# Kernel tuning notes

Hardware: AMD Instinct MI355X
Metric: run time of the kernel (lower is better)

## Reference

```python
import jax, jax.numpy as jnp
import numpy as np

ETA = 1.0
BETA = 0.6
LN_EPS = 1e-5


def layer_norm(x, scale, bias):
    mu = x.mean(-1, keepdims=True)
    var = ((x - mu) ** 2).mean(-1, keepdims=True)
    return (x - mu) / jnp.sqrt(var + LN_EPS) * scale + bias


def setup_inputs() -> dict:
    B, N, S, C, D = 8, 2048, 16, 32, 128
    key = jax.random.key(0)
    ks = jax.random.split(key, 10)
    X_short = jax.random.normal(ks[0], (B, N, S, C), dtype=jnp.float32)
    # binary temporal validity mask (float, as multiplied in the original)
    mask_short = (jax.random.uniform(ks[1], (B, N, S)) > 0.3).astype(jnp.float32)
    A_stat = jax.random.uniform(ks[2], (N, N), dtype=jnp.float32)
    M_mask = jax.random.randint(ks[3], (N, N), 0, 2).astype(jnp.int32)
    M_mask = M_mask.at[jnp.arange(N), jnp.arange(N)].set(1)  # keep self-edges so no all-masked row
    node_reliab = jax.random.uniform(ks[4], (B, N), dtype=jnp.float32)
    # learned parameters (stored (in, out) so application is x @ W)
    W_proj = jax.random.normal(ks[5], (C, D), dtype=jnp.float32) / np.sqrt(C)
    Wq = jax.random.normal(ks[6], (D, D), dtype=jnp.float32) / np.sqrt(D)
    Wk = jax.random.normal(ks[7], (D, D), dtype=jnp.float32) / np.sqrt(D)
    W_lin = jax.random.normal(ks[8], (D, D), dtype=jnp.float32) / np.sqrt(D)
    ln1_scale = jnp.ones((D,), jnp.float32)
    ln1_bias = jnp.zeros((D,), jnp.float32)
    ln2_scale = jnp.ones((D,), jnp.float32)
    ln2_bias = jnp.zeros((D,), jnp.float32)
    return {
        "X_short": X_short, "mask_short": mask_short, "A_stat": A_stat,
        "M_mask": M_mask, "node_reliab": node_reliab,
        "W_proj": W_proj, "Wq": Wq, "Wk": Wk, "W_lin": W_lin,
        "ln1_scale": ln1_scale, "ln1_bias": ln1_bias,
        "ln2_scale": ln2_scale, "ln2_bias": ln2_bias,
    }


def reference(X_short, mask_short, A_stat, M_mask, node_reliab,
              W_proj, Wq, Wk, W_lin, ln1_scale, ln1_bias, ln2_scale, ln2_bias):
    D = W_proj.shape[1]
    # masked temporal mean pooling over S
    denom = jnp.maximum(mask_short.sum(axis=2, keepdims=True), 1.0)      # (B,N,1)
    x = (X_short * mask_short[..., None]).sum(axis=2) / denom            # (B,N,C)
    Hn = x @ W_proj                                                      # (B,N,D)
    # dynamic graph attention
    Q = Hn @ Wq
    K = Hn @ Wk
    logits = jnp.einsum('bnd,bmd->bnm', Q, K) / jnp.sqrt(jnp.float32(D))
    p = jnp.clip(A_stat, 1e-3, 1.0 - 1e-3)
    bias = jnp.log(p / (1.0 - p))                                        # logit
    logits = logits + ETA * bias[None]
    edge = (M_mask != 0)[None]                                           # (1,N,N)
    logits = jnp.where(edge, logits, -jnp.inf)
    Adyn = jax.nn.softmax(logits, axis=-1)                               # (B,N,N)
    # fuse with static adjacency, reliability scaling, mask, row-renormalize
    A_fuse = BETA * Adyn + (1.0 - BETA) * A_stat[None]
    r = jnp.clip(node_reliab, 0.0, 1.0)                                  # (B,N)
    A_fuse = A_fuse * r[:, :, None] * r[:, None, :]
    A_fuse = A_fuse * M_mask.astype(A_fuse.dtype)[None]
    A_fuse = A_fuse / (A_fuse.sum(axis=-1, keepdims=True) + 1e-8)
    # propagate: A @ H -> linear -> relu -> (dropout=eval identity) -> LN -> outer LN
    H = jnp.einsum('bnm,bmd->bnd', A_fuse, Hn)
    H = H @ W_lin
    H = layer_norm(jax.nn.relu(H), ln1_scale, ln1_bias)
    out = layer_norm(H, ln2_scale, ln2_bias)
    return out, A_fuse
```

## Files before the change

### kernel.cpp

```cpp
#include <hip/hip_runtime.h>
#include <math.h>

#define BB 8
#define NN 2048
#define SS 16
#define CC 32
#define DD 128

typedef unsigned short u16;
typedef __attribute__((ext_vector_type(8))) short bf16x8;
typedef __attribute__((ext_vector_type(4))) float f32x4;

__device__ inline u16 f2bf(float f) {
    union { float f; unsigned u; } c; c.f = f;
    unsigned r = c.u + 0x7fff + ((c.u >> 16) & 1);
    return (u16)(r >> 16);
}
__device__ inline float bf2f(u16 h) {
    union { unsigned u; float f; } c; c.u = ((unsigned)h) << 16;
    return c.f;
}
__device__ inline u16 f2h(float f) {
    union { _Float16 h; u16 u; } c; c.h = (_Float16)f;
    return c.u;
}
__device__ inline float h2f(u16 u) {
    union { _Float16 h; u16 v; } c; c.v = u;
    return (float)c.h;
}
__device__ inline float clamp01(float v) { return fminf(fmaxf(v, 0.f), 1.f); }

__global__ __launch_bounds__(256) void prep_kernel(const float* __restrict__ Astat,
                                                   const int* __restrict__ Mm,
                                                   const float* __restrict__ Wproj,
                                                   const float* __restrict__ Wq,
                                                   const float* __restrict__ Wk,
                                                   const float* __restrict__ Wl,
                                                   u16* __restrict__ lgh,
                                                   u16* __restrict__ am,
                                                   float* __restrict__ Wpq,
                                                   float* __restrict__ Wpk,
                                                   u16* __restrict__ WlT) {
    int bx = blockIdx.x;
    if (bx < 4096) {
        size_t g = ((size_t)bx * 256 + threadIdx.x) * 4;
        float4 a4 = *(const float4*)&Astat[g];
        int4 m4 = *(const int4*)&Mm[g];
        float a[4] = {a4.x, a4.y, a4.z, a4.w};
        int mm[4] = {m4.x, m4.y, m4.z, m4.w};
        ushort4 lo, ao;
        u16 lg[4], ab[4];
#pragma unroll
        for (int j = 0; j < 4; ++j) {
            float p = fminf(fmaxf(a[j], 1e-3f), 1.f - 1e-3f);
            float l = __logf(p / (1.f - p));
            lg[j] = mm[j] ? f2h(l) : (u16)0xFC00;
            ab[j] = mm[j] ? f2bf(a[j]) : (u16)0;
        }
        lo.x = lg[0]; lo.y = lg[1]; lo.z = lg[2]; lo.w = lg[3];
        ao.x = ab[0]; ao.y = ab[1]; ao.z = ab[2]; ao.w = ab[3];
        *(ushort4*)&lgh[g] = lo;
        *(ushort4*)&am[g] = ao;
    } else if (bx < 4128) {
        int i = (bx - 4096) * 256 + threadIdx.x;
        int d = i & 127;
        int c = (i >> 7) & 31;
        int mat = i >> 12;
        const float* Wt = mat ? Wk : Wq;
        float acc = 0.f;
#pragma unroll 4
        for (int e = 0; e < DD; ++e)
            acc = fmaf(Wproj[c * DD + e], Wt[e * DD + d], acc);
        (mat ? Wpk : Wpq)[c * DD + d] = acc;
    } else {
        int i = (bx - 4128) * 256 + threadIdx.x;
        int dp = i >> 7, d = i & 127;
        WlT[dp * DD + d] = f2bf(Wl[d * DD + dp]);
    }
}

__global__ __launch_bounds__(256) void proj3_kernel(const float* __restrict__ X,
                                                    const float* __restrict__ Msk,
                                                    const float* __restrict__ Wproj,
                                                    const float* __restrict__ Wpq,
                                                    const float* __restrict__ Wpk,
                                                    u16* __restrict__ HnT,
                                                    u16* __restrict__ Qb,
                                                    u16* __restrict__ Kb) {
    __shared__ float wp[CC * DD], wq[CC * DD], wk[CC * DD];
    __shared__ float xs[CC * 36];
    int t = threadIdx.x;
    for (int i = t; i < CC * DD; i += 256) {
        wp[i] = Wproj[i];
        wq[i] = Wpq[i];
        wk[i] = Wpk[i];
    }
    int rbase = blockIdx.x * 32;
    {
        int row = t >> 3, cg = t & 7;
        const float* xrow = X + ((size_t)(rbase + row) * SS) * CC + cg * 4;
        const float* mrow = Msk + (size_t)(rbase + row) * SS;
        float4 acc = make_float4(0.f, 0.f, 0.f, 0.f);
        float msum = 0.f;
#pragma unroll
        for (int s = 0; s < SS; ++s) {
            float mv = mrow[s];
            float4 xv = *(const float4*)&xrow[s * CC];
            msum += mv;
            acc.x = fmaf(xv.x, mv, acc.x);
            acc.y = fmaf(xv.y, mv, acc.y);
            acc.z = fmaf(xv.z, mv, acc.z);
            acc.w = fmaf(xv.w, mv, acc.w);
        }
        float inv = 1.f / fmaxf(msum, 1.0f);
        xs[(cg * 4 + 0) * 36 + row] = acc.x * inv;
        xs[(cg * 4 + 1) * 36 + row] = acc.y * inv;
        xs[(cg * 4 + 2) * 36 + row] = acc.z * inv;
        xs[(cg * 4 + 3) * 36 + row] = acc.w * inv;
    }
    __syncthreads();

    int col = t & 127;
    int g = t >> 7;
    float ah[16], aq[16], ak[16];
#pragma unroll
    for (int i = 0; i < 16; ++i) { ah[i] = 0.f; aq[i] = 0.f; ak[i] = 0.f; }

#pragma unroll 4
    for (int k = 0; k < CC; ++k) {
        float wpv = wp[k * DD + col], wqv = wq[k * DD + col], wkv = wk[k * DD + col];
        const float4* xp = (const float4*)&xs[k * 36 + g * 16];
        float4 a0 = xp[0], a1 = xp[1], a2 = xp[2], a3 = xp[3];
        float xv[16] = {a0.x, a0.y, a0.z, a0.w, a1.x, a1.y, a1.z, a1.w,
                        a2.x, a2.y, a2.z, a2.w, a3.x, a3.y, a3.z, a3.w};
#pragma unroll
        for (int i = 0; i < 16; ++i) {
            ah[i] = fmaf(xv[i], wpv, ah[i]);
            aq[i] = fmaf(xv[i], wqv, aq[i]);
            ak[i] = fmaf(xv[i], wkv, ak[i]);
        }
    }
    const float scale = 0.08838834764831845f;
#pragma unroll
    for (int i = 0; i < 16; ++i) {
        size_t row = (size_t)(rbase + g * 16 + i);
        Qb[row * DD + col] = f2bf(aq[i] * scale);
        Kb[row * DD + col] = f2bf(ak[i]);
    }
    int b = rbase >> 11;
    int n0 = (rbase & (NN - 1)) + g * 16;
    u16* hp = HnT + (size_t)b * DD * NN + (size_t)col * NN + n0;
    unsigned pk[8];
#pragma unroll
    for (int i = 0; i < 8; ++i)
        pk[i] = (unsigned)f2bf(ah[2 * i]) | ((unsigned)f2bf(ah[2 * i + 1]) << 16);
    *(uint4*)&hp[0] = make_uint4(pk[0], pk[1], pk[2], pk[3]);
    *(uint4*)&hp[8] = make_uint4(pk[4], pk[5], pk[6], pk[7]);
}

#define LQT 136
__global__ __launch_bounds__(256) void stats_kernel(
        const u16* __restrict__ Qb, const u16* __restrict__ Kb,
        const u16* __restrict__ lgh, const u16* __restrict__ am,
        const float* __restrict__ rel,
        u16* __restrict__ Ebuf, float* __restrict__ part) {
    __shared__ u16 Qs[32 * LQT];
    __shared__ u16 Ks[128 * LQT];
    __shared__ float redE[128], redR[128], redA[128];
    int cs = blockIdx.x, rt = blockIdx.y, b = blockIdx.z;
    int R0 = rt * 32, C0 = cs * 512;
    int t = threadIdx.x;
    int lane = t & 63, w = t >> 6, q = lane >> 4, r16 = lane & 15;

    const u16* Qg = Qb + ((size_t)b * NN + R0) * DD;
#pragma unroll
    for (int rep = 0; rep < 2; ++rep) {
        int e = rep * 256 + t;
        int row = e >> 4, seg = e & 15;
        *(uint4*)&Qs[row * LQT + seg * 8] = *(const uint4*)&Qg[row * DD + seg * 8];
    }
    const u16* Kg = Kb + (size_t)b * NN * DD;
    float ER[2][4], LR[2][4], LA[2][4];
#pragma unroll
    for (int i = 0; i < 2; ++i)
#pragma unroll
        for (int r = 0; r < 4; ++r) { ER[i][r] = 0.f; LR[i][r] = 0.f; LA[i][r] = 0.f; }

    for (int ct = 0; ct < 4; ++ct) {
        __syncthreads();
#pragma unroll
        for (int rep = 0; rep < 8; ++rep) {
            int e = rep * 256 + t;
            int colr = e >> 4, seg = e & 15;
            *(uint4*)&Ks[colr * LQT + seg * 8] =
                *(const uint4*)&Kg[(size_t)(C0 + ct * 128 + colr) * DD + seg * 8];
        }
        __syncthreads();
        f32x4 acc[2][2];
#pragma unroll
        for (int i = 0; i < 2; ++i)
#pragma unroll
            for (int j = 0; j < 2; ++j)
                acc[i][j] = (f32x4){0.f, 0.f, 0.f, 0.f};
#pragma unroll
        for (int ksp = 0; ksp < 4; ++ksp) {
            int ko = ksp * 32 + q * 8;
            bf16x8 a0 = *(const bf16x8*)&Qs[r16 * LQT + ko];
            bf16x8 a1 = *(const bf16x8*)&Qs[(16 + r16) * LQT + ko];
            bf16x8 b0 = *(const bf16x8*)&Ks[(w * 32 + r16) * LQT + ko];
            bf16x8 b1 = *(const bf16x8*)&Ks[(w * 32 + 16 + r16) * LQT + ko];
            acc[0][0] = __builtin_amdgcn_mfma_f32_16x16x32_bf16(a0, b0, acc[0][0], 0, 0, 0);
            acc[0][1] = __builtin_amdgcn_mfma_f32_16x16x32_bf16(a0, b1, acc[0][1], 0, 0, 0);
            acc[1][0] = __builtin_amdgcn_mfma_f32_16x16x32_bf16(a1, b0, acc[1][0], 0, 0, 0);
            acc[1][1] = __builtin_amdgcn_mfma_f32_16x16x32_bf16(a1, b1, acc[1][1], 0, 0, 0);
        }
        int m0 = C0 + ct * 128 + w * 32;
        float rm0 = clamp01(rel[b * NN + m0 + r16]);
        float rm1 = clamp01(rel[b * NN + m0 + 16 + r16]);
#pragma unroll
        for (int i = 0; i < 2; ++i)
#pragma unroll
            for (int r = 0; r < 4; ++r) {
                int n = R0 + i * 16 + q * 4 + r;
                const u16* lrow = lgh + (size_t)n * NN + m0;
                const u16* arow = am + (size_t)n * NN + m0;
                float lg0 = h2f(lrow[r16]), lg1 = h2f(lrow[16 + r16]);
                float a0 = bf2f(arow[r16]), a1 = bf2f(arow[16 + r16]);
                u16 eb0 = f2bf(__expf(acc[i][0][r] + lg0));
                u16 eb1 = f2bf(__expf(acc[i][1][r] + lg1));
                size_t o = ((size_t)b * NN + n) * NN + m0;
                Ebuf[o + r16] = eb0;
                Ebuf[o + 16 + r16] = eb1;
                float e0 = bf2f(eb0), e1 = bf2f(eb1);
                ER[i][r] += e0 + e1;
                LR[i][r] = fmaf(e0, rm0, fmaf(e1, rm1, LR[i][r]));
                LA[i][r] = fmaf(a0, rm0, fmaf(a1, rm1, LA[i][r]));
            }
    }
#pragma unroll
    for (int i = 0; i < 2; ++i)
#pragma unroll
        for (int r = 0; r < 4; ++r) {
            float e = ER[i][r], lr = LR[i][r], la = LA[i][r];
#pragma unroll
            for (int off = 1; off < 16; off <<= 1) {
                e += __shfl_xor(e, off);
                lr += __shfl_xor(lr, off);
                la += __shfl_xor(la, off);
            }
            if (r16 == 0) {
                int row = i * 16 + q * 4 + r;
                redE[w * 32 + row] = e;
                redR[w * 32 + row] = lr;
                redA[w * 32 + row] = la;
            }
        }
    __syncthreads();
    if (t < 32) {
        float es = redE[t] + redE[32 + t] + redE[64 + t] + redE[96 + t];
        float lr = redR[t] + redR[32 + t] + redR[64 + t] + redR[96 + t];
        float la = redA[t] + redA[32 + t] + redA[64 + t] + redA[96 + t];
        float* p = part + ((size_t)((b * 64 + rt) * 4 + cs)) * 96;
        p[t] = es;
        p[32 + t] = lr;
        p[64 + t] = la;
    }
}

#define LPT 72
#define LWT 136
__global__ __launch_bounds__(512) void prop_kernel(
        const u16* __restrict__ Ebuf, const u16* __restrict__ am,
        const float* __restrict__ part, const float* __restrict__ rel,
        const u16* __restrict__ HnT, const u16* __restrict__ WlT,
        const float* __restrict__ s1, const float* __restrict__ b1,
        const float* __restrict__ s2, const float* __restrict__ b2,
        float* __restrict__ Af, float* __restrict__ out) {
    __shared__ union {
        struct { u16 As[32 * LPT]; u16 Bs[128 * LPT]; } ab;
        struct { u16 Ws[128 * LWT]; u16 Hs[32 * LWT]; } fin;
    } sm;
    __shared__ float redS[128], redQ[128];
    __shared__ float2 MV[32];
    __shared__ float2 cfs[32];
    int rt = blockIdx.x, b = blockIdx.y;
    int R0 = rt * 32;
    int t = threadIdx.x;
    int lane = t & 63, w = t >> 6, q = lane >> 4, r16 = lane & 15;
    int wr = (w >> 2) * 16;
    int wc = (w & 3) * 32;

    if (t < 32) {
        const float* p = part + ((size_t)((b * 64 + rt) * 4)) * 96;
        float es = 0.f, lr = 0.f, la = 0.f;
#pragma unroll
        for (int cs = 0; cs < 4; ++cs) {
            es += p[cs * 96 + t];
            lr += p[cs * 96 + 32 + t];
            la += p[cs * 96 + 64 + t];
        }
        float rn = clamp01(rel[b * NN + R0 + t]);
        float inv = 1.f / es;
        float fsum = rn * (0.6f * lr * inv + 0.4f * la);
        float nrm = 1.f / (fsum + 1e-8f);
        cfs[t] = make_float2(0.6f * inv * rn * nrm, 0.4f * rn * nrm);
    }
    __syncthreads();

    int arow = t >> 4, ac = (t & 15) * 4;
    float2 cf = cfs[arow];
    const u16* Eg = Ebuf + ((size_t)b * NN + R0 + arow) * NN;
    const u16* ag = am + (size_t)(R0 + arow) * NN;
    const float* rg = rel + b * NN;
    const u16* Bg = HnT + (size_t)b * DD * NN;
    float* Afg = Af + ((size_t)b * NN + R0 + arow) * NN;

    int bd0 = t >> 3, bs0 = (t & 7) * 8;
    int bd1 = (512 + t) >> 3, bs1 = bs0;

    f32x4 acc[2];
    acc[0] = (f32x4){0.f, 0.f, 0.f, 0.f};
    acc[1] = (f32x4){0.f, 0.f, 0.f, 0.f};

    uint2 pe = *(const uint2*)&Eg[ac];
    uint2 pa = *(const uint2*)&ag[ac];
    float4 pr = *(const float4*)&rg[ac];
    uint4 pb0 = *(const uint4*)&Bg[(size_t)bd0 * NN + bs0];
    uint4 pb1 = *(const uint4*)&Bg[(size_t)bd1 * NN + bs1];

    for (int kc = 0; kc < NN; kc += 64) {
        __syncthreads();
        {
            float e0 = bf2f((u16)(pe.x & 0xffff)), e1 = bf2f((u16)(pe.x >> 16));
            float e2 = bf2f((u16)(pe.y & 0xffff)), e3 = bf2f((u16)(pe.y >> 16));
            float a0 = bf2f((u16)(pa.x & 0xffff)), a1 = bf2f((u16)(pa.x >> 16));
            float a2 = bf2f((u16)(pa.y & 0xffff)), a3 = bf2f((u16)(pa.y >> 16));
            float r0 = clamp01(pr.x), r1 = clamp01(pr.y);
            float r2 = clamp01(pr.z), r3 = clamp01(pr.w);
            float v0 = r0 * fmaf(e0, cf.x, a0 * cf.y);
            float v1 = r1 * fmaf(e1, cf.x, a1 * cf.y);
            float v2 = r2 * fmaf(e2, cf.x, a2 * cf.y);
            float v3 = r3 * fmaf(e3, cf.x, a3 * cf.y);
            *(float4*)&Afg[kc + ac] = make_float4(v0, v1, v2, v3);
            unsigned pk0 = (unsigned)f2bf(v0) | ((unsigned)f2bf(v1) << 16);
            unsigned pk1 = (unsigned)f2bf(v2) | ((unsigned)f2bf(v3) << 16);
            *(uint2*)&sm.ab.As[arow * LPT + ac] = make_uint2(pk0, pk1);
        }
        *(uint4*)&sm.ab.Bs[bd0 * LPT + bs0] = pb0;
        *(uint4*)&sm.ab.Bs[bd1 * LPT + bs1] = pb1;
        if (kc + 64 < NN) {
            int kn = kc + 64;
            pe = *(const uint2*)&Eg[kn + ac];
            pa = *(const uint2*)&ag[kn + ac];
            pr = *(const float4*)&rg[kn + ac];
            pb0 = *(const uint4*)&Bg[(size_t)bd0 * NN + kn + bs0];
            pb1 = *(const uint4*)&Bg[(size_t)bd1 * NN + kn + bs1];
        }
        __syncthreads();
#pragma unroll
        for (int kst = 0; kst < 2; ++kst) {
            int ko = kst * 32 + q * 8;
            bf16x8 a0 = *(const bf16x8*)&sm.ab.As[(wr + r16) * LPT + ko];
            bf16x8 b0 = *(const bf16x8*)&sm.ab.Bs[(wc + r16) * LPT + ko];
            bf16x8 b1v = *(const bf16x8*)&sm.ab.Bs[(wc + 16 + r16) * LPT + ko];
            acc[0] = __builtin_amdgcn_mfma_f32_16x16x32_bf16(a0, b0, acc[0], 0, 0, 0);
            acc[1] = __builtin_amdgcn_mfma_f32_16x16x32_bf16(a0, b1v, acc[1], 0, 0, 0);
        }
    }

    __syncthreads();
#pragma unroll
    for (int rep = 0; rep < 4; ++rep) {
        int e = rep * 512 + t;
        int dp = e >> 4, seg = e & 15;
        *(uint4*)&sm.fin.Ws[dp * LWT + seg * 8] = *(const uint4*)&WlT[dp * DD + seg * 8];
    }
#pragma unroll
    for (int j = 0; j < 2; ++j)
#pragma unroll
        for (int r = 0; r < 4; ++r)
            sm.fin.Hs[(wr + q * 4 + r) * LWT + wc + j * 16 + r16] = f2bf(acc[j][r]);
    __syncthreads();

    f32x4 c2[2];
    c2[0] = (f32x4){0.f, 0.f, 0.f, 0.f};
    c2[1] = (f32x4){0.f, 0.f, 0.f, 0.f};
#pragma unroll
    for (int ksp = 0; ksp < 4; ++ksp) {
        int ko = ksp * 32 + q * 8;
        bf16x8 a0 = *(const bf16x8*)&sm.fin.Hs[(wr + r16) * LWT + ko];
        bf16x8 b0 = *(const bf16x8*)&sm.fin.Ws[(wc + r16) * LWT + ko];
        bf16x8 b1v = *(const bf16x8*)&sm.fin.Ws[(wc + 16 + r16) * LWT + ko];
        c2[0] = __builtin_amdgcn_mfma_f32_16x16x32_bf16(a0, b0, c2[0], 0, 0, 0);
        c2[1] = __builtin_amdgcn_mfma_f32_16x16x32_bf16(a0, b1v, c2[1], 0, 0, 0);
    }
    float v[2][4];
#pragma unroll
    for (int j = 0; j < 2; ++j)
#pragma unroll
        for (int r = 0; r < 4; ++r)
            v[j][r] = fmaxf(c2[j][r], 0.f);

    int c0 = wc + r16, c1 = wc + 16 + r16;
    float s1c0 = s1[c0], s1c1 = s1[c1], b1c0 = b1[c0], b1c1 = b1[c1];
    float s2c0 = s2[c0], s2c1 = s2[c1], b2c0 = b2[c0], b2c1 = b2[c1];
    int g4 = (w & 3) * 32;

#pragma unroll
    for (int r = 0; r < 4; ++r) {
        float s = v[0][r] + v[1][r];
        float qq = v[0][r] * v[0][r] + v[1][r] * v[1][r];
#pragma unroll
        for (int off = 1; off < 16; off <<= 1) {
            s += __shfl_xor(s, off);
            qq += __shfl_xor(qq, off);
        }
        if (r16 == 0) {
            int row = wr + q * 4 + r;
            redS[g4 + row] = s;
            redQ[g4 + row] = qq;
        }
    }
    __syncthreads();
    if (t < 32) {
        float s = redS[t] + redS[32 + t] + redS[64 + t] + redS[96 + t];
        float qq = redQ[t] + redQ[32 + t] + redQ[64 + t] + redQ[96 + t];
        float mu = s * (1.f / 128.f);
        float var = qq * (1.f / 128.f) - mu * mu;
        MV[t] = make_float2(mu, 1.f / sqrtf(var + 1e-5f));
    }
    __syncthreads();
    float y[2][4];
#pragma unroll
    for (int r = 0; r < 4; ++r) {
        float2 mv = MV[wr + q * 4 + r];
        y[0][r] = (v[0][r] - mv.x) * mv.y * s1c0 + b1c0;
        y[1][r] = (v[1][r] - mv.x) * mv.y * s1c1 + b1c1;
    }
    __syncthreads();
#pragma unroll
    for (int r = 0; r < 4; ++r) {
        float s = y[0][r] + y[1][r];
        float qq = y[0][r] * y[0][r] + y[1][r] * y[1][r];
#pragma unroll
        for (int off = 1; off < 16; off <<= 1) {
            s += __shfl_xor(s, off);
            qq += __shfl_xor(qq, off);
        }
        if (r16 == 0) {
            int row = wr + q * 4 + r;
            redS[g4 + row] = s;
            redQ[g4 + row] = qq;
        }
    }
    __syncthreads();
    if (t < 32) {
        float s = redS[t] + redS[32 + t] + redS[64 + t] + redS[96 + t];
        float qq = redQ[t] + redQ[32 + t] + redQ[64 + t] + redQ[96 + t];
        float mu = s * (1.f / 128.f);
        float var = qq * (1.f / 128.f) - mu * mu;
        MV[t] = make_float2(mu, 1.f / sqrtf(var + 1e-5f));
    }
    __syncthreads();
#pragma unroll
    for (int r = 0; r < 4; ++r) {
        float2 mv = MV[wr + q * 4 + r];
        size_t o = ((size_t)b * NN + R0 + wr + q * 4 + r) * DD;
        out[o + c0] = (y[0][r] - mv.x) * mv.y * s2c0 + b2c0;
        out[o + c1] = (y[1][r] - mv.x) * mv.y * s2c1 + b2c1;
    }
}

extern "C" void kernel_launch(void* const* d_in, const int* in_sizes, int n_in,
                              void* d_out, int out_size, void* d_ws, size_t ws_size,
                              hipStream_t stream) {
    const float* X = (const float*)d_in[0];
    const float* Msk = (const float*)d_in[1];
    const float* Astat = (const float*)d_in[2];
    const int* Mm = (const int*)d_in[3];
    const float* rel = (const float*)d_in[4];
    const float* Wproj = (const float*)d_in[5];
    const float* Wq = (const float*)d_in[6];
    const float* Wk = (const float*)d_in[7];
    const float* Wlin = (const float*)d_in[8];
    const float* s1 = (const float*)d_in[9];
    const float* b1 = (const float*)d_in[10];
    const float* s2 = (const float*)d_in[11];
    const float* b2 = (const float*)d_in[12];

    float* outMain = (float*)d_out;
    float* Afuse = outMain + (size_t)BB * NN * DD;

    float* w_ = (float*)d_ws;
    float* Wpq = w_;
    float* Wpk = w_ + 4096;
    u16* WlT = (u16*)(w_ + 8192);
    u16* Qb = (u16*)(w_ + 16384);
    u16* Kb = (u16*)(w_ + 1064960);
    u16* HnT = (u16*)(w_ + 2113536);
    u16* lgh = (u16*)(w_ + 3162112);
    u16* am = (u16*)(w_ + 5259264);
    u16* Ebuf = (u16*)(w_ + 7356416);
    float* part = w_ + 24133632;

    prep_kernel<<<dim3(4192), dim3(256), 0, stream>>>(
        Astat, Mm, Wproj, Wq, Wk, Wlin, lgh, am, Wpq, Wpk, WlT);
    proj3_kernel<<<dim3(512), dim3(256), 0, stream>>>(X, Msk, Wproj, Wpq, Wpk, HnT, Qb, Kb);

    stats_kernel<<<dim3(4, 64, 8), dim3(256), 0, stream>>>(
        Qb, Kb, lgh, am, rel, Ebuf, part);
    prop_kernel<<<dim3(64, 8), dim3(512), 0, stream>>>(
        Ebuf, am, part, rel, HnT, WlT, s1, b1, s2, b2, Afuse, outMain);
}
```

Before: 353.1 us.

## Recompute QK^T exponentials in prop kernel instead of storing Ebuf

Result: slower. 380.2 us (+7.7%).

```diff
diff --git a/kernel.cpp b/kernel.cpp
--- a/kernel.cpp
+++ b/kernel.cpp
@@ -163,12 +163,12 @@
         const u16* __restrict__ Qb, const u16* __restrict__ Kb,
         const u16* __restrict__ lgh, const u16* __restrict__ am,
         const float* __restrict__ rel,
-        u16* __restrict__ Ebuf, float* __restrict__ part) {
+        float2* __restrict__ coef) {
     __shared__ u16 Qs[32 * LQT];
     __shared__ u16 Ks[128 * LQT];
     __shared__ float redE[128], redR[128], redA[128];
-    int cs = blockIdx.x, rt = blockIdx.y, b = blockIdx.z;
-    int R0 = rt * 32, C0 = cs * 512;
+    int rt = blockIdx.x, b = blockIdx.y;
+    int R0 = rt * 32;
     int t = threadIdx.x;
     int lane = t & 63, w = t >> 6, q = lane >> 4, r16 = lane & 15;
 
@@ -186,14 +186,14 @@
 #pragma unroll
         for (int r = 0; r < 4; ++r) { ER[i][r] = 0.f; LR[i][r] = 0.f; LA[i][r] = 0.f; }
 
-    for (int ct = 0; ct < 4; ++ct) {
+    for (int ct = 0; ct < 16; ++ct) {
         __syncthreads();
 #pragma unroll
         for (int rep = 0; rep < 8; ++rep) {
             int e = rep * 256 + t;
             int colr = e >> 4, seg = e & 15;
             *(uint4*)&Ks[colr * LQT + seg * 8] =
-                *(const uint4*)&Kg[(size_t)(C0 + ct * 128 + colr) * DD + seg * 8];
+                *(const uint4*)&Kg[(size_t)(ct * 128 + colr) * DD + seg * 8];
         }
         __syncthreads();
         f32x4 acc[2][2];
@@ -214,7 +214,7 @@
             acc[1][0] = __builtin_amdgcn_mfma_f32_16x16x32_bf16(a1, b0, acc[1][0], 0, 0, 0);
             acc[1][1] = __builtin_amdgcn_mfma_f32_16x16x32_bf16(a1, b1, acc[1][1], 0, 0, 0);
         }
-        int m0 = C0 + ct * 128 + w * 32;
+        int m0 = ct * 128 + w * 32;
         float rm0 = clamp01(rel[b * NN + m0 + r16]);
         float rm1 = clamp01(rel[b * NN + m0 + 16 + r16]);
 #pragma unroll
@@ -226,12 +226,8 @@
                 const u16* arow = am + (size_t)n * NN + m0;
                 float lg0 = h2f(lrow[r16]), lg1 = h2f(lrow[16 + r16]);
                 float a0 = bf2f(arow[r16]), a1 = bf2f(arow[16 + r16]);
-                u16 eb0 = f2bf(__expf(acc[i][0][r] + lg0));
-                u16 eb1 = f2bf(__expf(acc[i][1][r] + lg1));
-                size_t o = ((size_t)b * NN + n) * NN + m0;
-                Ebuf[o + r16] = eb0;
-                Ebuf[o + 16 + r16] = eb1;
-                float e0 = bf2f(eb0), e1 = bf2f(eb1);
+                float e0 = __expf(acc[i][0][r] + lg0);
+                float e1 = __expf(acc[i][1][r] + lg1);
                 ER[i][r] += e0 + e1;
                 LR[i][r] = fmaf(e0, rm0, fmaf(e1, rm1, LR[i][r]));
                 LA[i][r] = fmaf(a0, rm0, fmaf(a1, rm1, LA[i][r]));
@@ -260,24 +256,27 @@
         float es = redE[t] + redE[32 + t] + redE[64 + t] + redE[96 + t];
         float lr = redR[t] + redR[32 + t] + redR[64 + t] + redR[96 + t];
         float la = redA[t] + redA[32 + t] + redA[64 + t] + redA[96 + t];
-        float* p = part + ((size_t)((b * 64 + rt) * 4 + cs)) * 96;
-        p[t] = es;
-        p[32 + t] = lr;
-        p[64 + t] = la;
+        float rn = clamp01(rel[b * NN + R0 + t]);
+        float inv = 1.f / es;
+        float fsum = rn * (0.6f * lr * inv + 0.4f * la);
+        float nrm = 1.f / (fsum + 1e-8f);
+        coef[b * NN + R0 + t] = make_float2(0.6f * inv * rn * nrm, 0.4f * rn * nrm);
     }
 }
 
 #define LPT 72
 #define LWT 136
 __global__ __launch_bounds__(512) void prop_kernel(
-        const u16* __restrict__ Ebuf, const u16* __restrict__ am,
-        const float* __restrict__ part, const float* __restrict__ rel,
+        const u16* __restrict__ Qb, const u16* __restrict__ Kb,
+        const u16* __restrict__ lgh, const u16* __restrict__ am,
+        const float2* __restrict__ coef, const float* __restrict__ rel,
         const u16* __restrict__ HnT, const u16* __restrict__ WlT,
         const float* __restrict__ s1, const float* __restrict__ b1,
         const float* __restrict__ s2, const float* __restrict__ b2,
         float* __restrict__ Af, float* __restrict__ out) {
     __shared__ union {
-        struct { u16 As[32 * LPT]; u16 Bs[128 * LPT]; } ab;
+        struct { u16 Qs[32 * LQT]; u16 Ks[64 * LQT];
+                 u16 Bs[128 * LPT]; u16 As[32 * LPT]; } ck;
         struct { u16 Ws[128 * LWT]; u16 Hs[32 * LWT]; } fin;
     } sm;
     __shared__ float redS[128], redQ[128];
@@ -287,82 +286,76 @@
     int R0 = rt * 32;
     int t = threadIdx.x;
     int lane = t & 63, w = t >> 6, q = lane >> 4, r16 = lane & 15;
-    int wr = (w >> 2) * 16;
-    int wc = (w & 3) * 32;
-
-    if (t < 32) {
-        const float* p = part + ((size_t)((b * 64 + rt) * 4)) * 96;
-        float es = 0.f, lr = 0.f, la = 0.f;
-#pragma unroll
-        for (int cs = 0; cs < 4; ++cs) {
-            es += p[cs * 96 + t];
-            lr += p[cs * 96 + 32 + t];
-            la += p[cs * 96 + 64 + t];
-        }
-        float rn = clamp01(rel[b * NN + R0 + t]);
-        float inv = 1.f / es;
-        float fsum = rn * (0.6f * lr * inv + 0.4f * la);
-        float nrm = 1.f / (fsum + 1e-8f);
-        cfs[t] = make_float2(0.6f * inv * rn * nrm, 0.4f * rn * nrm);
-    }
-    __syncthreads();
-
-    int arow = t >> 4, ac = (t & 15) * 4;
-    float2 cf = cfs[arow];
-    const u16* Eg = Ebuf + ((size_t)b * NN + R0 + arow) * NN;
-    const u16* ag = am + (size_t)(R0 + arow) * NN;
-    const float* rg = rel + b * NN;
+    int i2 = w >> 2, j2 = w & 3;
+    int wr = i2 * 16;
+    int wc = j2 * 32;
+
+    if (t < 32) cfs[t] = coef[b * NN + R0 + t];
+
+    const u16* Qg = Qb + ((size_t)b * NN + R0) * DD;
+    {
+        int row = t >> 4, seg = t & 15;
+        *(uint4*)&sm.ck.Qs[row * LQT + seg * 8] = *(const uint4*)&Qg[row * DD + seg * 8];
+    }
+
+    const u16* Kg = Kb + (size_t)b * NN * DD;
     const u16* Bg = HnT + (size_t)b * DD * NN;
-    float* Afg = Af + ((size_t)b * NN + R0 + arow) * NN;
-
-    int bd0 = t >> 3, bs0 = (t & 7) * 8;
-    int bd1 = (512 + t) >> 3, bs1 = bs0;
+    int krow0 = t >> 4, krow1 = 32 + (t >> 4), kseg = (t & 15) * 8;
+    int bd0 = t >> 3, bd1 = 64 + (t >> 3), bsg = (t & 7) * 8;
 
     f32x4 acc[2];
     acc[0] = (f32x4){0.f, 0.f, 0.f, 0.f};
     acc[1] = (f32x4){0.f, 0.f, 0.f, 0.f};
 
-    uint2 pe = *(const uint2*)&Eg[ac];
-    uint2 pa = *(const uint2*)&ag[ac];
-    float4 pr = *(const float4*)&rg[ac];
-    uint4 pb0 = *(const uint4*)&Bg[(size_t)bd0 * NN + bs0];
-    uint4 pb1 = *(const uint4*)&Bg[(size_t)bd1 * NN + bs1];
+    uint4 pk0 = *(const uint4*)&Kg[(size_t)krow0 * DD + kseg];
+    uint4 pk1 = *(const uint4*)&Kg[(size_t)krow1 * DD + kseg];
+    uint4 pb0 = *(const uint4*)&Bg[(size_t)bd0 * NN + bsg];
+    uint4 pb1 = *(const uint4*)&Bg[(size_t)bd1 * NN + bsg];
 
     for (int kc = 0; kc < NN; kc += 64) {
         __syncthreads();
-        {
-            float e0 = bf2f((u16)(pe.x & 0xffff)), e1 = bf2f((u16)(pe.x >> 16));
-            float e2 = bf2f((u16)(pe.y & 0xffff)), e3 = bf2f((u16)(pe.y >> 16));
-            float a0 = bf2f((u16)(pa.x & 0xffff)), a1 = bf2f((u16)(pa.x >> 16));
-            float a2 = bf2f((u16)(pa.y & 0xffff)), a3 = bf2f((u16)(pa.y >> 16));
-            float r0 = clamp01(pr.x), r1 = clamp01(pr.y);
-            float r2 = clamp01(pr.z), r3 = clamp01(pr.w);
-            float v0 = r0 * fmaf(e0, cf.x, a0 * cf.y);
-            float v1 = r1 * fmaf(e1, cf.x, a1 * cf.y);
-            float v2 = r2 * fmaf(e2, cf.x, a2 * cf.y);
-            float v3 = r3 * fmaf(e3, cf.x, a3 * cf.y);
-            *(float4*)&Afg[kc + ac] = make_float4(v0, v1, v2, v3);
-            unsigned pk0 = (unsigned)f2bf(v0) | ((unsigned)f2bf(v1) << 16);
-            unsigned pk1 = (unsigned)f2bf(v2) | ((unsigned)f2bf(v3) << 16);
-            *(uint2*)&sm.ab.As[arow * LPT + ac] = make_uint2(pk0, pk1);
-        }
-        *(uint4*)&sm.ab.Bs[bd0 * LPT + bs0] = pb0;
-        *(uint4*)&sm.ab.Bs[bd1 * LPT + bs1] = pb1;
+        *(uint4*)&sm.ck.Ks[krow0 * LQT + kseg] = pk0;
+        *(uint4*)&sm.ck.Ks[krow1 * LQT + kseg] = pk1;
+        *(uint4*)&sm.ck.Bs[bd0 * LPT + bsg] = pb0;
+        *(uint4*)&sm.ck.Bs[bd1 * LPT + bsg] = pb1;
         if (kc + 64 < NN) {
             int kn = kc + 64;
-            pe = *(const uint2*)&Eg[kn + ac];
-            pa = *(const uint2*)&ag[kn + ac];
-            pr = *(const float4*)&rg[kn + ac];
-            pb0 = *(const uint4*)&Bg[(size_t)bd0 * NN + kn + bs0];
-            pb1 = *(const uint4*)&Bg[(size_t)bd1 * NN + kn + bs1];
+            pk0 = *(const uint4*)&Kg[(size_t)(kn + krow0) * DD + kseg];
+            pk1 = *(const uint4*)&Kg[(size_t)(kn + krow1) * DD + kseg];
+            pb0 = *(const uint4*)&Bg[(size_t)bd0 * NN + kn + bsg];
+            pb1 = *(const uint4*)&Bg[(size_t)bd1 * NN + kn + bsg];
+        }
+        __syncthreads();
+        f32x4 sa = (f32x4){0.f, 0.f, 0.f, 0.f};
+#pragma unroll
+        for (int ksp = 0; ksp < 4; ++ksp) {
+            int ko = ksp * 32 + q * 8;
+            bf16x8 a0 = *(const bf16x8*)&sm.ck.Qs[(wr + r16) * LQT + ko];
+            bf16x8 b0 = *(const bf16x8*)&sm.ck.Ks[(j2 * 16 + r16) * LQT + ko];
+            sa = __builtin_amdgcn_mfma_f32_16x16x32_bf16(a0, b0, sa, 0, 0, 0);
+        }
+        int mloc = j2 * 16 + r16;
+        int mb = kc + mloc;
+        float rm = clamp01(rel[b * NN + mb]);
+#pragma unroll
+        for (int r = 0; r < 4; ++r) {
+            int nl = wr + q * 4 + r;
+            int n = R0 + nl;
+            float lg = h2f(lgh[(size_t)n * NN + mb]);
+            float av = bf2f(am[(size_t)n * NN + mb]);
+            float2 cf = cfs[nl];
+            float e = __expf(sa[r] + lg);
+            float v = rm * fmaf(e, cf.x, av * cf.y);
+            Af[((size_t)b * NN + n) * NN + mb] = v;
+            sm.ck.As[nl * LPT + mloc] = f2bf(v);
         }
         __syncthreads();
 #pragma unroll
         for (int kst = 0; kst < 2; ++kst) {
             int ko = kst * 32 + q * 8;
-            bf16x8 a0 = *(const bf16x8*)&sm.ab.As[(wr + r16) * LPT + ko];
-            bf16x8 b0 = *(const bf16x8*)&sm.ab.Bs[(wc + r16) * LPT + ko];
-            bf16x8 b1v = *(const bf16x8*)&sm.ab.Bs[(wc + 16 + r16) * LPT + ko];
+            bf16x8 a0 = *(const bf16x8*)&sm.ck.As[(wr + r16) * LPT + ko];
+            bf16x8 b0 = *(const bf16x8*)&sm.ck.Bs[(wc + r16) * LPT + ko];
+            bf16x8 b1v = *(const bf16x8*)&sm.ck.Bs[(wc + 16 + r16) * LPT + ko];
             acc[0] = __builtin_amdgcn_mfma_f32_16x16x32_bf16(a0, b0, acc[0], 0, 0, 0);
             acc[1] = __builtin_amdgcn_mfma_f32_16x16x32_bf16(a0, b1v, acc[1], 0, 0, 0);
         }
@@ -500,15 +493,14 @@
     u16* HnT = (u16*)(w_ + 2113536);
     u16* lgh = (u16*)(w_ + 3162112);
     u16* am = (u16*)(w_ + 5259264);
-    u16* Ebuf = (u16*)(w_ + 7356416);
-    float* part = w_ + 24133632;
+    float2* coef = (float2*)(w_ + 7356416);
 
     prep_kernel<<<dim3(4192), dim3(256), 0, stream>>>(
         Astat, Mm, Wproj, Wq, Wk, Wlin, lgh, am, Wpq, Wpk, WlT);
     proj3_kernel<<<dim3(512), dim3(256), 0, stream>>>(X, Msk, Wproj, Wpq, Wpk, HnT, Qb, Kb);
 
-    stats_kernel<<<dim3(4, 64, 8), dim3(256), 0, stream>>>(
-        Qb, Kb, lgh, am, rel, Ebuf, part);
+    stats_kernel<<<dim3(64, 8), dim3(256), 0, stream>>>(
+        Qb, Kb, lgh, am, rel, coef);
     prop_kernel<<<dim3(64, 8), dim3(512), 0, stream>>>(
-        Ebuf, am, part, rel, HnT, WlT, s1, b1, s2, b2, Afuse, outMain);
-}
+        Qb, Kb, lgh, am, coef, rel, HnT, WlT, s1, b1, s2, b2, Afuse, outMain);
+}
```
